# Performance work log

Measured on AMD Instinct MI355X. Metric: run time of the kernel, lower is better.

Reference implementation:

```python
import jax, jax.numpy as jnp
from jax import lax
import numpy as np

B, T, C_IN, H, W = 2, 4, 128, 64, 64
D_MODEL, N_Q, N_POINTS, PATCH, N_LAYERS = 256, 300, 8, 3, 6


def _sine_pos(Hh, Ww, d, temperature=10000.0):
    # mask is all-False, so cumsum of ones -> arange(1..H)/H * 2pi
    two_pi = 2.0 * np.pi
    yn = (jnp.arange(1, Hh + 1, dtype=jnp.float32) / (Hh + 1e-6)) * two_pi
    xn = (jnp.arange(1, Ww + 1, dtype=jnp.float32) / (Ww + 1e-6)) * two_pi
    q = d // 4
    i = jnp.arange(q, dtype=jnp.float32)
    dim_t = temperature ** (2.0 * jnp.floor(i / 2.0) / q)
    py = yn[:, None] / dim_t
    px = xn[:, None] / dim_t
    py = jnp.stack([jnp.sin(py), jnp.cos(py)], axis=-1).reshape(Hh, 2 * q)
    px = jnp.stack([jnp.sin(px), jnp.cos(px)], axis=-1).reshape(Ww, 2 * q)
    pos = jnp.concatenate([
        jnp.broadcast_to(py[:, None, :], (Hh, Ww, 2 * q)),
        jnp.broadcast_to(px[None, :, :], (Hh, Ww, 2 * q)),
    ], axis=-1)
    return jnp.transpose(pos, (2, 0, 1))  # [d,H,W]


def _sample_scale(fmap, ref, ps):
    # fmap [B,C,h,w]; ref [B,nQ,nP,2] in [0,1]. Bilinear grid_sample,
    # padding_mode='border', align_corners=True -> direct gather (no replication).
    Bc, C, h, w = fmap.shape
    half = (ps - 1) / 2.0
    off = jnp.linspace(-half, half, ps, dtype=jnp.float32)
    oy, ox = jnp.meshgrid(off, off, indexing='ij')  # [ps,ps]
    gx = ref[..., 0, None, None] * 2.0 - 1.0 + ox * (2.0 / w)  # [B,nQ,nP,ps,ps]
    gy = ref[..., 1, None, None] * 2.0 - 1.0 + oy * (2.0 / h)
    x = jnp.clip((gx + 1.0) * 0.5 * (w - 1), 0.0, w - 1.0)
    y = jnp.clip((gy + 1.0) * 0.5 * (h - 1), 0.0, h - 1.0)
    x0 = jnp.floor(x); y0 = jnp.floor(y)
    wx = x - x0; wy = y - y0
    x0i = x0.astype(jnp.int32); y0i = y0.astype(jnp.int32)
    x1i = jnp.minimum(x0i + 1, w - 1); y1i = jnp.minimum(y0i + 1, h - 1)

    def per_b(fb, y0b, x0b, y1b, x1b, wxb, wyb):
        v00 = fb[:, y0b, x0b]  # [C,nQ,nP,ps,ps]
        v01 = fb[:, y0b, x1b]
        v10 = fb[:, y1b, x0b]
        v11 = fb[:, y1b, x1b]
        return (v00 * (1 - wxb) * (1 - wyb) + v01 * wxb * (1 - wyb)
                + v10 * (1 - wxb) * wyb + v11 * wxb * wyb)

    out = jax.vmap(per_b)(fmap, y0i, x0i, y1i, x1i, wx, wy)  # [B,C,nQ,nP,ps,ps]
    return jnp.transpose(out, (0, 2, 3, 4, 5, 1))  # [B,nQ,nP,ps,ps,C]


def reference(feat, pred_boxes_init, w_tf, b_tf, w_in, b_in, w_lat, b_lat, w_sm, b_sm,
              q_embed, q_pos, Wq, bq, Wo, bo, Wp1, bp1, Wp2, bp2,
              w_r1, b_r1, w_r2, b_r2, w_b1, b_b1, w_b2, b_b2, w_cls, b_cls):
    Bb, Tt, Cin, Hh, Ww = feat.shape
    d = w_in.shape[0]
    nP = w_r2.shape[0] // 2
    ps = int(round((Wp1.shape[-1] // d) ** 0.5))
    # temporal fuse: Conv3d kernel (3,1,1), padding (1,0,0)
    x = lax.conv_general_dilated(jnp.transpose(feat, (0, 2, 1, 3, 4)), w_tf,
                                 (1, 1, 1), [(1, 1), (0, 0), (0, 0)],
                                 dimension_numbers=('NCDHW', 'OIDHW', 'NCDHW'))
    x = x + b_tf[None, :, None, None, None]
    x = x.mean(axis=2)  # [B,Cin,H,W]
    x = jnp.einsum('bchw,dc->bdhw', x, w_in) + b_in[None, :, None, None]
    x = x + _sine_pos(Hh, Ww, d)[None]
    # FPN over scales {1,2,4}: avg_pool -> 1x1 lateral -> 3x3 smooth
    feats = []
    for i, s in enumerate((1, 2, 4)):
        xi = x if s == 1 else x.reshape(Bb, d, Hh // s, s, Ww // s, s).mean(axis=(3, 5))
        xi = jnp.einsum('bchw,oc->bohw', xi, w_lat[i]) + b_lat[i][None, :, None, None]
        xi = lax.conv_general_dilated(xi, w_sm[i], (1, 1), [(1, 1), (1, 1)],
                                      dimension_numbers=('NCHW', 'OIHW', 'NCHW'))
        xi = xi + b_sm[i][None, :, None, None]
        feats.append(xi)
    nQ = q_embed.shape[0]
    queries = jnp.broadcast_to((q_embed + q_pos)[None], (Bb, nQ, d))
    boxes = pred_boxes_init
    inv_sqrt_d = 1.0 / float(np.sqrt(d))
    for l in range(Wq.shape[0]):
        h1 = jax.nn.relu(jnp.einsum('bqd,od->bqo', queries, w_r1) + b_r1)
        ro = jnp.tanh(jnp.einsum('bqd,od->bqo', h1, w_r2) + b_r2)
        ro = ro.reshape(Bb, nQ, nP, 2) * 0.5
        ref = jnp.clip(boxes[:, :, None, :2] + ro, 0.0, 1.0)
        sampled = jnp.concatenate([_sample_scale(f, ref, ps) for f in feats], axis=2)
        sampled = sampled[:, :, :nP]  # truncate multi-scale concat back to nP
        flat = sampled.reshape(Bb, nQ, nP, ps * ps * d)
        pv = jax.nn.relu(jnp.einsum('bqpi,oi->bqpo', flat, Wp1[l]) + bp1[l])
        pv = jnp.einsum('bqpd,od->bqpo', pv, Wp2[l]) + bp2[l]
        kv = pv.mean(axis=2)  # [B,nP_q,d] -> [B,nQ,d]
        q = jnp.einsum('bqd,od->bqo', queries, Wq[l]) + bq[l]
        attn = jax.nn.softmax(jnp.einsum('bqd,bkd->bqk', q, kv) * inv_sqrt_d, axis=-1)
        out = jnp.einsum('bqk,bkd->bqd', attn, kv)
        queries = queries + (jnp.einsum('bqd,od->bqo', out, Wo[l]) + bo[l])
        hb = jax.nn.relu(jnp.einsum('bqd,od->bqo', queries, w_b1) + b_b1)
        delta = jax.nn.sigmoid(jnp.einsum('bqd,od->bqo', hb, w_b2) + b_b2)
        boxes = jnp.clip(boxes + 0.1 * jnp.tanh(delta - 0.5), 0.0, 1.0)
    logits = (jnp.einsum('bqd,od->bqo', queries, w_cls) + b_cls)[..., 0]
    return logits, boxes


def setup_inputs() -> dict:
    key = jax.random.key(0)
    keys = iter(jax.random.split(key, 48))

    def nrm(shape, s=0.02):
        return jax.random.normal(next(keys), shape, dtype=jnp.float32) * s

    inp = {
        'feat': jax.random.normal(next(keys), (B, T, C_IN, H, W), dtype=jnp.float32),
        'pred_boxes_init': jax.random.uniform(next(keys), (B, N_Q, 4), dtype=jnp.float32),
        'w_tf': nrm((C_IN, C_IN, 3, 1, 1)), 'b_tf': jnp.zeros((C_IN,), jnp.float32),
        'w_in': nrm((D_MODEL, C_IN)), 'b_in': jnp.zeros((D_MODEL,), jnp.float32),
        'w_lat': nrm((3, D_MODEL, D_MODEL)), 'b_lat': jnp.zeros((3, D_MODEL), jnp.float32),
        'w_sm': nrm((3, D_MODEL, D_MODEL, 3, 3)), 'b_sm': jnp.zeros((3, D_MODEL), jnp.float32),
        'q_embed': nrm((N_Q, D_MODEL), 1.0), 'q_pos': nrm((N_Q, D_MODEL), 1.0),
        'Wq': nrm((N_LAYERS, D_MODEL, D_MODEL)), 'bq': jnp.zeros((N_LAYERS, D_MODEL), jnp.float32),
        'Wo': nrm((N_LAYERS, D_MODEL, D_MODEL)), 'bo': jnp.zeros((N_LAYERS, D_MODEL), jnp.float32),
        'Wp1': nrm((N_LAYERS, D_MODEL, PATCH * PATCH * D_MODEL)), 'bp1': jnp.zeros((N_LAYERS, D_MODEL), jnp.float32),
        'Wp2': nrm((N_LAYERS, D_MODEL, D_MODEL)), 'bp2': jnp.zeros((N_LAYERS, D_MODEL), jnp.float32),
        'w_r1': nrm((D_MODEL, D_MODEL)), 'b_r1': jnp.zeros((D_MODEL,), jnp.float32),
        'w_r2': nrm((2 * N_POINTS, D_MODEL)), 'b_r2': jnp.zeros((2 * N_POINTS,), jnp.float32),
        'w_b1': nrm((D_MODEL, D_MODEL)), 'b_b1': jnp.zeros((D_MODEL,), jnp.float32),
        'w_b2': nrm((4, D_MODEL)), 'b_b2': jnp.zeros((4,), jnp.float32),
        'w_cls': nrm((1, D_MODEL)), 'b_cls': jnp.zeros((1,), jnp.float32),
    }
    return inp
```

## Files before the change

kernel.cpp:

```cpp
#include <hip/hip_runtime.h>
#include <hip/hip_bf16.h>
#include <math.h>

#define BB 2
#define TT 4
#define CIN 128
#define DM 256
#define NQ 300
#define NP 8
#define PS 3
#define NL 6
#define HW 4096
#define KP 2304

typedef __attribute__((ext_vector_type(8))) short short8;
typedef __attribute__((ext_vector_type(4))) short short4_t;
typedef __attribute__((ext_vector_type(4))) float f32x4;
typedef unsigned short ushort_t;

static __device__ __forceinline__ ushort_t f2bf(float f) {
  __hip_bfloat16 h = __float2bfloat16(f);
  return *reinterpret_cast<ushort_t*>(&h);
}
static __device__ __forceinline__ float bf2f(ushort_t u) {
  return __uint_as_float(((unsigned)u) << 16);
}

__global__ void k_prep(const float* __restrict__ w_in, const float* __restrict__ w_lat,
                       const float* __restrict__ w_b1,
                       const float* __restrict__ w_r1, const float* __restrict__ Wp1,
                       ushort_t* __restrict__ win_bf, ushort_t* __restrict__ wlat_bf,
                       ushort_t* __restrict__ wb1_bf,
                       ushort_t* __restrict__ wr1_bf, ushort_t* __restrict__ wp1_bf,
                       const float* __restrict__ w_tf, ushort_t* __restrict__ tct,
                       const float* __restrict__ w_sm, ushort_t* __restrict__ wsm_bf,
                       const float* __restrict__ Wp2, const float* __restrict__ Wo,
                       const float* __restrict__ bq, const float* __restrict__ bp2,
                       const float* __restrict__ bo,
                       float* __restrict__ bqt, float* __restrict__ bfuse,
                       uint4* __restrict__ x2p_zero,
                       const float* __restrict__ b_tf, const float* __restrict__ b_in,
                       float* __restrict__ bias_comb,
                       const float* __restrict__ qe, const float* __restrict__ qp,
                       const float* __restrict__ pb, float* __restrict__ queries,
                       ushort_t* __restrict__ qbf, float* __restrict__ boxes,
                       const float* __restrict__ feat, ushort_t* __restrict__ featT) {
  __shared__ float ldsF[64][65];
  float* bt = &ldsF[0][0];
  int b = blockIdx.x, t = threadIdx.x;
  if (b < 3680) {
    int i = b * 256 + t;
    const float* s; ushort_t* d; int base;
    if (i < 8192)         { s = w_in;  d = win_bf;  base = 0; }
    else if (i < 24576)   { s = w_lat; d = wlat_bf; base = 8192; }
    else if (i < 40960)   { s = w_b1;  d = wb1_bf;  base = 24576; }
    else if (i < 57344)   { s = w_r1;  d = wr1_bf;  base = 40960; }
    else                  { s = Wp1;   d = wp1_bf;  base = 57344; }
    int j = i - base;
    float4 v = ((const float4*)s)[j];
    short4_t o;
    o[0] = (short)f2bf(v.x); o[1] = (short)f2bf(v.y);
    o[2] = (short)f2bf(v.z); o[3] = (short)f2bf(v.w);
    *(short4_t*)(d + j * 4) = o;
  } else if (b < 3936) {
    int i = (b - 3680) * 256 + t;
    int k = i >> 7, c = i & 127;
    int u = k >> 7, ci = k & 127;
    const float* wp = w_tf + ((size_t)(c * 128 + ci)) * 3;
    float w0 = wp[0], w1 = wp[1], w2 = wp[2];
    float coef = (u == 0) ? (w0 + w1) : (u == 3) ? (w1 + w2) : (w0 + w1 + w2);
    tct[(size_t)k * 128 + c] = f2bf(0.25f * coef);
  } else if (b < 4192) {
    int n = b - 3936;
    float* l2 = &ldsF[0][0];
    const float* src = w_sm + (size_t)n * KP;
    for (int idx = t; idx < 576; idx += 256) {
      float4 v = ((const float4*)src)[idx];
      l2[idx * 4 + 0] = v.x; l2[idx * 4 + 1] = v.y;
      l2[idx * 4 + 2] = v.z; l2[idx * 4 + 3] = v.w;
    }
    __syncthreads();
    ushort_t* dst = wsm_bf + (size_t)n * KP;
#pragma unroll
    for (int tp = 0; tp < 9; ++tp)
      dst[tp * 256 + t] = f2bf(l2[t * 9 + tp]);
  } else if (b < 4204) {
    int i = (b - 4192) * 256 + t;
    if (i < 1536) {
      int l = i >> 8, d = i & 255;
      float a = 0.f;
      for (int o = 0; o < 256; ++o)
        a += bq[l * 256 + o] * Wp2[((size_t)(l * 256 + o)) * 256 + d];
      bqt[i] = a;
    } else {
      int j = i - 1536;
      int l = j >> 8, o2 = j & 255;
      float a = bo[l * 256 + o2];
      for (int o = 0; o < 256; ++o)
        a += bp2[l * 256 + o] * Wo[((size_t)(l * 256 + o2)) * 256 + o];
      bfuse[j] = a;
    }
  } else if (b < 5293) {
    int j = (b - 4204) * 256 + t;
    if (j < 278784) x2p_zero[j] = make_uint4(0u, 0u, 0u, 0u);
  } else if (b < 5294) {
    int d = t;
    if (d < 128) bt[d] = b_tf[d];
    __syncthreads();
    float a = b_in[d];
    for (int c = 0; c < 128; ++c) a += w_in[d * 128 + c] * bt[c];
    bias_comb[d] = a;
  } else if (b < 5894) {
    int i = (b - 5294) * 256 + t;
    if (i < BB * NQ * DM) {
      int rd = i % (NQ * DM);
      float v = qe[rd] + qp[rd];
      queries[i] = v;
      qbf[i] = f2bf(v);
    }
    if (i < BB * NQ * 4) boxes[i] = pb[i];
  } else {
    int idx = b - 5894;
    int gs = idx & 127;
    int k0 = (idx >> 7) * 64;
    int bb = gs >> 6;
    int s0 = (gs & 63) * 64;
    int kk = t >> 2, sc0 = (t & 3) * 16;
    {
      int k = k0 + kk;
      int u = k >> 7, ci = k & 127;
      const float* src = feat + (((size_t)(bb * 4 + u) * 128 + ci) << 12) + s0 + sc0;
#pragma unroll
      for (int j = 0; j < 4; ++j) {
        float4 v = *(const float4*)(src + j * 4);
        ldsF[kk][sc0 + j * 4 + 0] = v.x;
        ldsF[kk][sc0 + j * 4 + 1] = v.y;
        ldsF[kk][sc0 + j * 4 + 2] = v.z;
        ldsF[kk][sc0 + j * 4 + 3] = v.w;
      }
    }
    __syncthreads();
#pragma unroll
    for (int p = 0; p < 2; ++p) {
      int idx2 = p * 256 + t;
      int s_l = idx2 >> 3, kc = (idx2 & 7) * 8;
      short8 v;
#pragma unroll
      for (int j = 0; j < 8; ++j) v[j] = (short)f2bf(ldsF[kc + j][s_l]);
      *(short8*)(featT + (size_t)(bb * 4096 + s0 + s_l) * 512 + k0 + kc) = v;
    }
  }
}

__global__ __launch_bounds__(256) void k_wcompose(const float* __restrict__ Wp2,
                                                  const float* __restrict__ Wq,
                                                  const float* __restrict__ Wo,
                                                  ushort_t* __restrict__ wqt,
                                                  ushort_t* __restrict__ wfuseT) {
  __shared__ ushort_t As[64 * 36];
  __shared__ ushort_t Bs[64 * 36];
  int z = blockIdx.z, l = z % 6;
  const float* Asrc = Wp2 + (size_t)l * 65536;
  const float* Bsrc = ((z < 6) ? Wq : Wo) + (size_t)l * 65536;
  ushort_t* C = ((z < 6) ? wqt : wfuseT) + (size_t)l * 65536;
  bool btr = (z < 6);
  int tid = threadIdx.x;
  int bm = blockIdx.x * 64, bn = blockIdx.y * 64;
  int w = tid >> 6, lane = tid & 63;
  int wm = (w & 1) * 32, wn = (w >> 1) * 32;
  int q = lane >> 4, ml = lane & 15;
  f32x4 acc[2][2] = {};
  int oo = tid >> 3, mg = (tid & 7) * 8;
  int nr = tid >> 2, kg = (tid & 3) * 8;
  for (int k0 = 0; k0 < 256; k0 += 32) {
    {
      const float* sp = Asrc + (size_t)(k0 + oo) * 256 + bm + mg;
      float4 f0 = *(const float4*)sp;
      float4 f1 = *(const float4*)(sp + 4);
      ushort_t* dst = As + oo;
      dst[(mg + 0) * 36] = f2bf(f0.x); dst[(mg + 1) * 36] = f2bf(f0.y);
      dst[(mg + 2) * 36] = f2bf(f0.z); dst[(mg + 3) * 36] = f2bf(f0.w);
      dst[(mg + 4) * 36] = f2bf(f1.x); dst[(mg + 5) * 36] = f2bf(f1.y);
      dst[(mg + 6) * 36] = f2bf(f1.z); dst[(mg + 7) * 36] = f2bf(f1.w);
    }
    if (btr) {
      const float* sp = Bsrc + (size_t)(k0 + oo) * 256 + bn + mg;
      float4 f0 = *(const float4*)sp;
      float4 f1 = *(const float4*)(sp + 4);
      ushort_t* dst = Bs + oo;
      dst[(mg + 0) * 36] = f2bf(f0.x); dst[(mg + 1) * 36] = f2bf(f0.y);
      dst[(mg + 2) * 36] = f2bf(f0.z); dst[(mg + 3) * 36] = f2bf(f0.w);
      dst[(mg + 4) * 36] = f2bf(f1.x); dst[(mg + 5) * 36] = f2bf(f1.y);
      dst[(mg + 6) * 36] = f2bf(f1.z); dst[(mg + 7) * 36] = f2bf(f1.w);
    } else {
      const float* sp = Bsrc + (size_t)(bn + nr) * 256 + k0 + kg;
      float4 f0 = *(const float4*)sp;
      float4 f1 = *(const float4*)(sp + 4);
      short8 v;
      v[0] = (short)f2bf(f0.x); v[1] = (short)f2bf(f0.y);
      v[2] = (short)f2bf(f0.z); v[3] = (short)f2bf(f0.w);
      v[4] = (short)f2bf(f1.x); v[5] = (short)f2bf(f1.y);
      v[6] = (short)f2bf(f1.z); v[7] = (short)f2bf(f1.w);
      *(short8*)(Bs + nr * 36 + kg) = v;
    }
    __syncthreads();
    short8 a0 = *(const short8*)(As + (wm + ml) * 36 + q * 8);
    short8 a1 = *(const short8*)(As + (wm + 16 + ml) * 36 + q * 8);
    short8 b0 = *(const short8*)(Bs + (wn + ml) * 36 + q * 8);
    short8 b1 = *(const short8*)(Bs + (wn + 16 + ml) * 36 + q * 8);
    acc[0][0] = __builtin_amdgcn_mfma_f32_16x16x32_bf16(a0, b0, acc[0][0], 0, 0, 0);
    acc[0][1] = __builtin_amdgcn_mfma_f32_16x16x32_bf16(a0, b1, acc[0][1], 0, 0, 0);
    acc[1][0] = __builtin_amdgcn_mfma_f32_16x16x32_bf16(a1, b0, acc[1][0], 0, 0, 0);
    acc[1][1] = __builtin_amdgcn_mfma_f32_16x16x32_bf16(a1, b1, acc[1][1], 0, 0, 0);
    __syncthreads();
  }
#pragma unroll
  for (int i = 0; i < 2; ++i)
#pragma unroll
    for (int j = 0; j < 2; ++j) {
      int cn = bn + wn + j * 16 + ml;
#pragma unroll
      for (int r = 0; r < 4; ++r) {
        int rm = bm + wm + i * 16 + q * 4 + r;
        C[(size_t)rm * 256 + cn] = f2bf(acc[i][j][r]);
      }
    }
}

__global__ __launch_bounds__(256) void k_feat2(const ushort_t* __restrict__ featT,
                                               const ushort_t* __restrict__ wcomb,
                                               const float* __restrict__ biasc,
                                               ushort_t* __restrict__ xcl) {
  __shared__ ushort_t As[32 * 72];
  __shared__ ushort_t Bs[64 * 72];
  __shared__ float dimt_s[256];
  int tid = threadIdx.x;
  {
    int dd = tid & 127;
    int ii = dd >> 1;
    dimt_s[tid] = powf(10000.0f, (2.0f * (float)(ii >> 1)) / 64.0f);
  }
  int bm = blockIdx.x * 32, bn = blockIdx.y * 64;
  int w = tid >> 6, lane = tid & 63;
  int wm = (w & 1) * 16, wn = (w >> 1) * 32;
  int q = lane >> 4, ml = lane & 15;
  int sra = tid >> 3, sca = (tid & 7) * 8;
  int srb = tid >> 2, scb = (tid & 3) * 16;
  const ushort_t* Ag = featT + (size_t)(bm + sra) * 512 + sca;
  const ushort_t* Wg = wcomb + (size_t)(bn + srb) * 512 + scb;
  f32x4 acc[2] = {};
  short8 av = *(const short8*)Ag;
  short8 wv0 = *(const short8*)Wg;
  short8 wv1 = *(const short8*)(Wg + 8);
  for (int k0 = 0; k0 < 512; k0 += 64) {
    *(short8*)(As + sra * 72 + sca) = av;
    *(short8*)(Bs + srb * 72 + scb) = wv0;
    *(short8*)(Bs + srb * 72 + scb + 8) = wv1;
    __syncthreads();
    if (k0 + 64 < 512) {
      av = *(const short8*)(Ag + k0 + 64);
      wv0 = *(const short8*)(Wg + k0 + 64);
      wv1 = *(const short8*)(Wg + k0 + 72);
    }
#pragma unroll
    for (int h = 0; h < 2; ++h) {
      int kc = h * 32 + q * 8;
      short8 a = *(const short8*)(As + (wm + ml) * 72 + kc);
      short8 b0 = *(const short8*)(Bs + (wn + ml) * 72 + kc);
      short8 b1 = *(const short8*)(Bs + (wn + 16 + ml) * 72 + kc);
      acc[0] = __builtin_amdgcn_mfma_f32_16x16x32_bf16(a, b0, acc[0], 0, 0, 0);
      acc[1] = __builtin_amdgcn_mfma_f32_16x16x32_bf16(a, b1, acc[1], 0, 0, 0);
    }
    __syncthreads();
  }
  const float FKT = 6.28318530717958647692f / 64.000001f;
#pragma unroll
  for (int j = 0; j < 2; ++j) {
    int cn = bn + wn + j * 16 + ml;
    float dimt = dimt_s[cn];
    float bC = biasc[cn];
    bool isx = cn >= 128;
    bool isc = cn & 1;
#pragma unroll
    for (int r = 0; r < 4; ++r) {
      int rm = bm + wm + q * 4 + r;
      int s = rm & 4095;
      int y = s >> 6, x = s & 63;
      float ang = (float)((isx ? x : y) + 1) * FKT / dimt;
      float pos = isc ? cosf(ang) : sinf(ang);
      xcl[(size_t)rm * 256 + cn] = f2bf(acc[j][r] + bC + pos);
    }
  }
}

template <int ACT, int OUTMODE, int MG>
__global__ __launch_bounds__(256) void k_gemm_bf16(const ushort_t* __restrict__ A,
                                                   const ushort_t* __restrict__ W,
                                                   const float* __restrict__ bias,
                                                   const float* __restrict__ res,
                                                   float* __restrict__ Cf,
                                                   ushort_t* __restrict__ Cb,
                                                   int M, int N, int K) {
  __shared__ ushort_t As[64 * 72];
  __shared__ ushort_t Bs[64 * 72];
  int tid = threadIdx.x;
  int bm = blockIdx.x * 64, bn = blockIdx.y * 64;
  int w = tid >> 6, lane = tid & 63;
  int wm = (w & 1) * 32, wn = (w >> 1) * 32;
  int q = lane >> 4, ml = lane & 15;
  f32x4 acc[2][2] = {};
  int srow = tid >> 2, scol = (tid & 3) * 16;
  int ga = bm + srow;
  if (MG) ga = min(ga, M - 1);
  const ushort_t* Ag = A + (size_t)ga * K + scol;
  const ushort_t* Wg = W + (size_t)(bn + srow) * K + scol;
  short8 av0 = *(const short8*)(Ag);
  short8 av1 = *(const short8*)(Ag + 8);
  short8 wv0 = *(const short8*)(Wg);
  short8 wv1 = *(const short8*)(Wg + 8);
  for (int k0 = 0; k0 < K; k0 += 64) {
    *(short8*)(As + srow * 72 + scol) = av0;
    *(short8*)(As + srow * 72 + scol + 8) = av1;
    *(short8*)(Bs + srow * 72 + scol) = wv0;
    *(short8*)(Bs + srow * 72 + scol + 8) = wv1;
    __syncthreads();
    if (k0 + 64 < K) {
      av0 = *(const short8*)(Ag + k0 + 64);
      av1 = *(const short8*)(Ag + k0 + 72);
      wv0 = *(const short8*)(Wg + k0 + 64);
      wv1 = *(const short8*)(Wg + k0 + 72);
    }
#pragma unroll
    for (int h = 0; h < 2; ++h) {
      int kc = h * 32 + q * 8;
      short8 a0 = *(const short8*)(As + (wm + ml) * 72 + kc);
      short8 a1 = *(const short8*)(As + (wm + 16 + ml) * 72 + kc);
      short8 b0 = *(const short8*)(Bs + (wn + ml) * 72 + kc);
      short8 b1 = *(const short8*)(Bs + (wn + 16 + ml) * 72 + kc);
      acc[0][0] = __builtin_amdgcn_mfma_f32_16x16x32_bf16(a0, b0, acc[0][0], 0, 0, 0);
      acc[0][1] = __builtin_amdgcn_mfma_f32_16x16x32_bf16(a0, b1, acc[0][1], 0, 0, 0);
      acc[1][0] = __builtin_amdgcn_mfma_f32_16x16x32_bf16(a1, b0, acc[1][0], 0, 0, 0);
      acc[1][1] = __builtin_amdgcn_mfma_f32_16x16x32_bf16(a1, b1, acc[1][1], 0, 0, 0);
    }
    __syncthreads();
  }
#pragma unroll
  for (int i = 0; i < 2; ++i) {
#pragma unroll
    for (int j = 0; j < 2; ++j) {
      int cn = bn + wn + j * 16 + ml;
      float bsv = bias ? bias[cn] : 0.f;
#pragma unroll
      for (int r = 0; r < 4; ++r) {
        int rm = bm + wm + i * 16 + q * 4 + r;
        if (MG && rm >= M) continue;
        float v = acc[i][j][r] + bsv;
        if (OUTMODE == 0) {
          if (ACT == 1) v = fmaxf(v, 0.f);
          Cf[(size_t)rm * N + cn] = v;
        } else if (OUTMODE == 1) {
          int b = rm >> 12, rem = rm & 4095;
          int y = rem >> 6, xx = rem & 63;
          Cb[(((size_t)(b * 66 + y + 1)) * 66 + xx + 1) * 256 + cn] = f2bf(v);
        } else if (OUTMODE == 6) {
          Cb[(size_t)rm * N + cn] = f2bf(v);
        }
      }
    }
  }
}

template <int OUTMODE>
__global__ __launch_bounds__(256) void k_gemm32(const ushort_t* __restrict__ A,
                                                const ushort_t* __restrict__ W,
                                                const float* __restrict__ bias,
                                                const float* __restrict__ res,
                                                float* __restrict__ Cf,
                                                ushort_t* __restrict__ Cb,
                                                int M, int K,
                                                const ushort_t* __restrict__ W2,
                                                const float* __restrict__ bias2,
                                                const ushort_t* __restrict__ W3,
                                                const float* __restrict__ bias3) {
  __shared__ ushort_t As[32 * 72];
  __shared__ ushort_t Bs[64 * 72];
  int tid = threadIdx.x;
  int bm = blockIdx.x * 32, bn = blockIdx.y * 64;
  int w = tid >> 6, lane = tid & 63;
  int wm = (w & 1) * 16, wn = (w >> 1) * 32;
  int q = lane >> 4, ml = lane & 15;
  int sra = tid >> 3, sca = (tid & 7) * 8;
  int srb = tid >> 2, scb = (tid & 3) * 16;
  int ga = min(bm + sra, M - 1);
  const ushort_t* Ag = A + (size_t)ga * K + sca;
  const ushort_t* Wg;
  if (OUTMODE == 7) {
    int seg = bn >> 8;
    const ushort_t* Wb = (seg == 0) ? W : ((seg == 1) ? W2 : W3);
    Wg = Wb + (size_t)((bn & 255) + srb) * K + scb;
  } else {
    const ushort_t* Wb = (bn < 256) ? W : W2;
    Wg = Wb + (size_t)((bn & 255) + srb) * K + scb;
  }
  f32x4 acc[2] = {};
  short8 av = *(const short8*)(Ag);
  short8 wv0 = *(const short8*)(Wg);
  short8 wv1 = *(const short8*)(Wg + 8);
  for (int k0 = 0; k0 < K; k0 += 64) {
    *(short8*)(As + sra * 72 + sca) = av;
    *(short8*)(Bs + srb * 72 + scb) = wv0;
    *(short8*)(Bs + srb * 72 + scb + 8) = wv1;
    __syncthreads();
    if (k0 + 64 < K) {
      av = *(const short8*)(Ag + k0 + 64);
      wv0 = *(const short8*)(Wg + k0 + 64);
      wv1 = *(const short8*)(Wg + k0 + 72);
    }
#pragma unroll
    for (int h = 0; h < 2; ++h) {
      int kc = h * 32 + q * 8;
      short8 a = *(const short8*)(As + (wm + ml) * 72 + kc);
      short8 b0 = *(const short8*)(Bs + (wn + ml) * 72 + kc);
      short8 b1 = *(const short8*)(Bs + (wn + 16 + ml) * 72 + kc);
      acc[0] = __builtin_amdgcn_mfma_f32_16x16x32_bf16(a, b0, acc[0], 0, 0, 0);
      acc[1] = __builtin_amdgcn_mfma_f32_16x16x32_bf16(a, b1, acc[1], 0, 0, 0);
    }
    __syncthreads();
  }
#pragma unroll
  for (int j = 0; j < 2; ++j) {
    int cn = bn + wn + j * 16 + ml;
    float bsv;
    if (OUTMODE == 7) {
      int seg = cn >> 8;
      bsv = ((seg == 0) ? bias : ((seg == 1) ? bias2 : bias3))[cn & 255];
    } else {
      bsv = ((cn < 256) ? bias : bias2)[cn & 255];
    }
#pragma unroll
    for (int r = 0; r < 4; ++r) {
      int rm = bm + wm + q * 4 + r;
      if (rm >= M) continue;
      float v = acc[j][r] + bsv;
      if (OUTMODE == 4) {
        if (cn < 256) Cf[(size_t)rm * 256 + cn] = fmaxf(v, 0.f);
        else Cb[(size_t)rm * 256 + (cn & 255)] = f2bf(v);
      } else {
        if (cn < 256) Cf[(size_t)rm * 256 + cn] = fmaxf(v, 0.f);
        else if (cn < 512) ((float*)Cb)[(size_t)rm * 256 + (cn & 255)] = fmaxf(v, 0.f);
        else ((ushort_t*)res)[(size_t)rm * 256 + (cn & 255)] = f2bf(v);
      }
    }
  }
}

__global__ __launch_bounds__(512) void k_wp1_split(const ushort_t* __restrict__ A,
                                                   const ushort_t* __restrict__ W,
                                                   ushort_t* __restrict__ part) {
  __shared__ ushort_t As[64 * 72];
  __shared__ ushort_t Bs[128 * 72];
  int tid = threadIdx.x;
  int bm = blockIdx.x * 64, bn = blockIdx.y * 128;
  int kz = blockIdx.z * 768;
  int w = tid >> 6, lane = tid & 63;
  int wm = (w & 1) * 32, wn = (w >> 1) * 32;
  int q = lane >> 4, ml = lane & 15;
  int srA = tid >> 3, scA = (tid & 7) * 8;
  int srB = tid >> 2, scB = (tid & 3) * 16;
  const ushort_t* Ag = A + (size_t)(bm + srA) * KP + kz + scA;
  const ushort_t* Wg = W + (size_t)(bn + srB) * KP + kz + scB;
  f32x4 acc[2][2] = {};
  short8 av = *(const short8*)(Ag);
  short8 wv0 = *(const short8*)(Wg);
  short8 wv1 = *(const short8*)(Wg + 8);
  for (int k0 = 0; k0 < 768; k0 += 64) {
    *(short8*)(As + srA * 72 + scA) = av;
    *(short8*)(Bs + srB * 72 + scB) = wv0;
    *(short8*)(Bs + srB * 72 + scB + 8) = wv1;
    __syncthreads();
    if (k0 + 64 < 768) {
      av = *(const short8*)(Ag + k0 + 64);
      wv0 = *(const short8*)(Wg + k0 + 64);
      wv1 = *(const short8*)(Wg + k0 + 72);
    }
#pragma unroll
    for (int h = 0; h < 2; ++h) {
      int kc = h * 32 + q * 8;
      short8 a0 = *(const short8*)(As + (wm + ml) * 72 + kc);
      short8 a1 = *(const short8*)(As + (wm + 16 + ml) * 72 + kc);
      short8 b0 = *(const short8*)(Bs + (wn + ml) * 72 + kc);
      short8 b1 = *(const short8*)(Bs + (wn + 16 + ml) * 72 + kc);
      acc[0][0] = __builtin_amdgcn_mfma_f32_16x16x32_bf16(a0, b0, acc[0][0], 0, 0, 0);
      acc[0][1] = __builtin_amdgcn_mfma_f32_16x16x32_bf16(a0, b1, acc[0][1], 0, 0, 0);
      acc[1][0] = __builtin_amdgcn_mfma_f32_16x16x32_bf16(a1, b0, acc[1][0], 0, 0, 0);
      acc[1][1] = __builtin_amdgcn_mfma_f32_16x16x32_bf16(a1, b1, acc[1][1], 0, 0, 0);
    }
    __syncthreads();
  }
  ushort_t* pz = part + (size_t)blockIdx.z * 4800 * 256;
#pragma unroll
  for (int i = 0; i < 2; ++i)
#pragma unroll
    for (int j = 0; j < 2; ++j) {
      int cn = bn + wn + j * 16 + ml;
#pragma unroll
      for (int r = 0; r < 4; ++r) {
        int rm = bm + wm + i * 16 + q * 4 + r;
        pz[(size_t)rm * 256 + cn] = f2bf(acc[i][j][r]);
      }
    }
}

__global__ __launch_bounds__(256) void k_wp1_reduce(const ushort_t* __restrict__ part,
                                                    const float* __restrict__ bias,
                                                    ushort_t* __restrict__ pvm) {
  int row = blockIdx.x;
  int d = threadIdx.x;
  float b = bias[d];
  float s = 0.f;
#pragma unroll
  for (int p = 0; p < 8; ++p) {
    size_t idx = (size_t)(row * 8 + p) * 256 + d;
    float v = bf2f(part[idx]) + bf2f(part[idx + (size_t)4800 * 256]) +
              bf2f(part[idx + (size_t)2 * 4800 * 256]) + b;
    s += fmaxf(v, 0.f);
  }
  pvm[(size_t)row * 256 + d] = f2bf(s * 0.125f);
}

__global__ __launch_bounds__(256) void k_conv3(const ushort_t* __restrict__ x2p,
                                               const ushort_t* __restrict__ wsm,
                                               const float* __restrict__ bsm,
                                               ushort_t* __restrict__ fcl) {
  __shared__ ushort_t As[32 * 72];
  __shared__ ushort_t Bs[64 * 72];
  int tid = threadIdx.x;
  int bm = blockIdx.x * 32, bn = blockIdx.y * 64;
  int w = tid >> 6, lane = tid & 63;
  int wm = (w & 1) * 16, wn = (w >> 1) * 32;
  int q = lane >> 4, ml = lane & 15;
  int sra = tid >> 3, sca = (tid & 7) * 8;
  int srb = tid >> 2, scb = (tid & 3) * 16;
  int sA = bm + sra;
  int b = sA >> 12, rem = sA & 4095;
  size_t pbase = ((size_t)(b * 66 + (rem >> 6)) * 66 + (rem & 63)) * 256;
  const ushort_t* Wg = wsm + (size_t)(bn + srb) * KP + scb;
  auto loadA = [&](int k0) {
    int ka = k0 + sca;
    int t9 = ka >> 8;
    int ky = t9 / 3, kx = t9 - ky * 3;
    return *(const short8*)(x2p + pbase + (size_t)(ky * 66 + kx) * 256 + (ka & 255));
  };
  f32x4 acc[2] = {};
  short8 av = loadA(0);
  short8 wv0 = *(const short8*)(Wg);
  short8 wv1 = *(const short8*)(Wg + 8);
  for (int k0 = 0; k0 < KP; k0 += 64) {
    *(short8*)(As + sra * 72 + sca) = av;
    *(short8*)(Bs + srb * 72 + scb) = wv0;
    *(short8*)(Bs + srb * 72 + scb + 8) = wv1;
    __syncthreads();
    if (k0 + 64 < KP) {
      av = loadA(k0 + 64);
      wv0 = *(const short8*)(Wg + k0 + 64);
      wv1 = *(const short8*)(Wg + k0 + 72);
    }
#pragma unroll
    for (int h = 0; h < 2; ++h) {
      int kc = h * 32 + q * 8;
      short8 a = *(const short8*)(As + (wm + ml) * 72 + kc);
      short8 b0 = *(const short8*)(Bs + (wn + ml) * 72 + kc);
      short8 b1 = *(const short8*)(Bs + (wn + 16 + ml) * 72 + kc);
      acc[0] = __builtin_amdgcn_mfma_f32_16x16x32_bf16(a, b0, acc[0], 0, 0, 0);
      acc[1] = __builtin_amdgcn_mfma_f32_16x16x32_bf16(a, b1, acc[1], 0, 0, 0);
    }
    __syncthreads();
  }
#pragma unroll
  for (int j = 0; j < 2; ++j) {
    int cn = bn + wn + j * 16 + ml;
    float bsv = bsm[cn];
#pragma unroll
    for (int r = 0; r < 4; ++r) {
      int rm = bm + wm + q * 4 + r;
      fcl[(size_t)rm * 256 + cn] = f2bf(acc[j][r] + bsv);
    }
  }
}

__global__ __launch_bounds__(256) void k_sample(const ushort_t* __restrict__ fcl,
                                                const float* __restrict__ h1,
                                                const float* __restrict__ w_r2,
                                                const float* __restrict__ b_r2,
                                                const float* __restrict__ boxesIn,
                                                float* __restrict__ boxesOut,
                                                const float* __restrict__ hb,
                                                const float* __restrict__ w_b2,
                                                const float* __restrict__ b_b2,
                                                ushort_t* __restrict__ flat) {
  __shared__ float pr[8];
  __shared__ float bc2[2];
  __shared__ float nb2[2];
  int blk = blockIdx.x;
  int row = blk >> 3, p = blk & 7;
  int b = row / NQ;
  int tid = threadIdx.x;
  int w = tid >> 6, lane = tid & 63;
  if (hb) {
    float4 hv = *(const float4*)(hb + (size_t)row * 256 + lane * 4);
    float4 wv = *(const float4*)(w_b2 + (size_t)w * 256 + lane * 4);
    float aa = hv.x * wv.x + hv.y * wv.y + hv.z * wv.z + hv.w * wv.w;
#pragma unroll
    for (int s = 32; s > 0; s >>= 1) aa += __shfl_down(aa, s, 64);
    if (lane == 0) {
      aa += b_b2[w];
      float delta = 1.0f / (1.0f + expf(-aa));
      float v = boxesIn[row * 4 + w] + 0.1f * tanhf(delta - 0.5f);
      v = fminf(fmaxf(v, 0.f), 1.f);
      if (w < 2) nb2[w] = v;
      if (p == 0) boxesOut[row * 4 + w] = v;
    }
  } else if (tid < 2) {
    nb2[tid] = boxesIn[row * 4 + tid];
  }
  float h = h1[(size_t)row * 256 + tid];
  float px = h * w_r2[(size_t)(2 * p) * 256 + tid];
  float py = h * w_r2[(size_t)(2 * p + 1) * 256 + tid];
#pragma unroll
  for (int s = 32; s > 0; s >>= 1) {
    px += __shfl_down(px, s, 64);
    py += __shfl_down(py, s, 64);
  }
  if (lane == 0) { pr[w * 2] = px; pr[w * 2 + 1] = py; }
  __syncthreads();
  if (tid == 0) {
    float sx = pr[0] + pr[2] + pr[4] + pr[6] + b_r2[2 * p];
    float sy = pr[1] + pr[3] + pr[5] + pr[7] + b_r2[2 * p + 1];
    float rx = nb2[0] + 0.5f * tanhf(sx);
    float ry = nb2[1] + 0.5f * tanhf(sy);
    bc2[0] = fminf(fmaxf(rx, 0.f), 1.f);
    bc2[1] = fminf(fmaxf(ry, 0.f), 1.f);
  }
  __syncthreads();
  float rx = bc2[0], ry = bc2[1];
  const ushort_t* fb = fcl + (size_t)b * HW * DM;
  ushort_t* op = flat + (size_t)blk * KP;
  int c4 = (tid & 63) * 4;
  int g = tid >> 6;
  int p0 = (g == 0) ? 0 : (1 + 2 * g);
  int p1 = (g == 0) ? 3 : (3 + 2 * g);
  for (int p9 = p0; p9 < p1; ++p9) {
    int jy = (p9 >= 6) ? 2 : ((p9 >= 3) ? 1 : 0);
    int jx = p9 - jy * 3;
    float yy = (ry + (float)(jy - 1) * (1.0f / 64.0f)) * 63.0f;
    yy = fminf(fmaxf(yy, 0.f), 63.0f);
    float y0f = floorf(yy);
    float wy = yy - y0f;
    int y0 = (int)y0f;
    int y1 = min(y0 + 1, 63);
    float xx = (rx + (float)(jx - 1) * (1.0f / 64.0f)) * 63.0f;
    xx = fminf(fmaxf(xx, 0.f), 63.0f);
    float x0f = floorf(xx);
    float wx = xx - x0f;
    int x0 = (int)x0f;
    int x1 = min(x0 + 1, 63);
    short4_t v00 = *(const short4_t*)(fb + (y0 * 64 + x0) * DM + c4);
    short4_t v01 = *(const short4_t*)(fb + (y0 * 64 + x1) * DM + c4);
    short4_t v10 = *(const short4_t*)(fb + (y1 * 64 + x0) * DM + c4);
    short4_t v11 = *(const short4_t*)(fb + (y1 * 64 + x1) * DM + c4);
    short4_t ov;
#pragma unroll
    for (int jj = 0; jj < 4; ++jj) {
      float v = bf2f((ushort_t)v00[jj]) * (1.f - wx) * (1.f - wy) +
                bf2f((ushort_t)v01[jj]) * wx * (1.f - wy) +
                bf2f((ushort_t)v10[jj]) * (1.f - wx) * wy +
                bf2f((ushort_t)v11[jj]) * wx * wy;
      ov[jj] = (short)f2bf(v);
    }
    *(short4_t*)(op + p9 * DM + c4) = ov;
  }
}

__global__ __launch_bounds__(256) void k_attn(const ushort_t* __restrict__ qt,
                                              const ushort_t* __restrict__ pvm,
                                              const ushort_t* __restrict__ wfT,
                                              const float* __restrict__ bfuse_l,
                                              float* __restrict__ queries,
                                              ushort_t* __restrict__ qbf) {
  __shared__ float qs[256];
  __shared__ float sc[512];
  __shared__ float red[256];
  __shared__ float pr4[1024];
  int row = blockIdx.x;
  int b = row / NQ;
  int tid = threadIdx.x;
  qs[tid] = bf2f(qt[(size_t)row * DM + tid]);
  __syncthreads();
  const ushort_t* kvB = pvm + (size_t)b * NQ * DM;
#pragma unroll
  for (int s2 = 0; s2 < 2; ++s2) {
    int k = tid + s2 * 256;
    float v = -1e30f;
    if (k < NQ) {
      const ushort_t* kp = kvB + (size_t)k * DM;
      float a = 0.f;
#pragma unroll
      for (int d = 0; d < 256; d += 8) {
        short8 k8 = *(const short8*)(kp + d);
        const float* qd = qs + d;
        a += bf2f((ushort_t)k8[0]) * qd[0];
        a += bf2f((ushort_t)k8[1]) * qd[1];
        a += bf2f((ushort_t)k8[2]) * qd[2];
        a += bf2f((ushort_t)k8[3]) * qd[3];
        a += bf2f((ushort_t)k8[4]) * qd[4];
        a += bf2f((ushort_t)k8[5]) * qd[5];
        a += bf2f((ushort_t)k8[6]) * qd[6];
        a += bf2f((ushort_t)k8[7]) * qd[7];
      }
      v = a * (1.0f / 16.0f);
    }
    sc[k] = v;
  }
  __syncthreads();
  red[tid] = fmaxf(sc[tid], sc[tid + 256]);
  __syncthreads();
  for (int st = 128; st > 0; st >>= 1) {
    if (tid < st) red[tid] = fmaxf(red[tid], red[tid + st]);
    __syncthreads();
  }
  float mx = red[0];
  __syncthreads();
  float e0 = (tid < NQ) ? expf(sc[tid] - mx) : 0.f;
  float e1 = (tid + 256 < NQ) ? expf(sc[tid + 256] - mx) : 0.f;
  sc[tid] = e0;
  sc[tid + 256] = e1;
  red[tid] = e0 + e1;
  __syncthreads();
  for (int st = 128; st > 0; st >>= 1) {
    if (tid < st) red[tid] += red[tid + st];
    __syncthreads();
  }
  float inv = 1.0f / red[0];
  __syncthreads();
  float acc = 0.f;
#pragma unroll 4
  for (int k = 0; k < NQ; ++k)
    acc += sc[k] * bf2f(kvB[(size_t)k * DM + tid]);
  qs[tid] = acc * inv;
  __syncthreads();
  int oq = (tid & 63) * 4, dq = (tid >> 6) * 64;
  float a0 = 0.f, a1 = 0.f, a2 = 0.f, a3 = 0.f;
  const ushort_t* wp = wfT + (size_t)dq * 256 + oq;
#pragma unroll 8
  for (int dd = 0; dd < 64; ++dd) {
    float cc = qs[dq + dd];
    short4_t wv = *(const short4_t*)(wp + (size_t)dd * 256);
    a0 += cc * bf2f((ushort_t)wv[0]);
    a1 += cc * bf2f((ushort_t)wv[1]);
    a2 += cc * bf2f((ushort_t)wv[2]);
    a3 += cc * bf2f((ushort_t)wv[3]);
  }
  float* pb4 = pr4 + (tid >> 6) * 256 + oq;
  pb4[0] = a0; pb4[1] = a1; pb4[2] = a2; pb4[3] = a3;
  __syncthreads();
  float v = pr4[tid] + pr4[256 + tid] + pr4[512 + tid] + pr4[768 + tid] +
            bfuse_l[tid] + queries[(size_t)row * DM + tid];
  queries[(size_t)row * DM + tid] = v;
  qbf[(size_t)row * DM + tid] = f2bf(v);
}

__global__ __launch_bounds__(256) void k_boxf(const float* __restrict__ hb,
                                              const float* __restrict__ w_b2,
                                              const float* __restrict__ b_b2,
                                              float* __restrict__ boxes,
                                              int last,
                                              const float* __restrict__ queries,
                                              const float* __restrict__ w_cls,
                                              const float* __restrict__ b_cls,
                                              float* __restrict__ out) {
  __shared__ float nb[4];
  int row = blockIdx.x;
  int tid = threadIdx.x;
  int j = tid >> 6, lane = tid & 63;
  float4 hv = *(const float4*)(hb + (size_t)row * 256 + lane * 4);
  float4 wv = *(const float4*)(w_b2 + (size_t)j * 256 + lane * 4);
  float aa = hv.x * wv.x + hv.y * wv.y + hv.z * wv.z + hv.w * wv.w;
#pragma unroll
  for (int s = 32; s > 0; s >>= 1) aa += __shfl_down(aa, s, 64);
  if (lane == 0) {
    aa += b_b2[j];
    float delta = 1.0f / (1.0f + expf(-aa));
    float v = boxes[row * 4 + j] + 0.1f * tanhf(delta - 0.5f);
    v = fminf(fmaxf(v, 0.f), 1.f);
    boxes[row * 4 + j] = v;
    nb[j] = v;
  }
  if (last) {
    __syncthreads();
    if (j == 0) {
      float4 qv = *(const float4*)(queries + (size_t)row * 256 + lane * 4);
      float4 cv = *(const float4*)(w_cls + lane * 4);
      float a2 = qv.x * cv.x + qv.y * cv.y + qv.z * cv.z + qv.w * cv.w;
#pragma unroll
      for (int s = 32; s > 0; s >>= 1) a2 += __shfl_down(a2, s, 64);
      if (lane == 0) out[row] = a2 + b_cls[0];
    } else if (j == 1 && lane < 4) {
      out[600 + row * 4 + lane] = nb[lane];
    }
  }
}

extern "C" void kernel_launch(void* const* d_in, const int* in_sizes, int n_in,
                              void* d_out, int out_size, void* d_ws, size_t ws_size,
                              hipStream_t stream) {
  const float* feat   = (const float*)d_in[0];
  const float* pb     = (const float*)d_in[1];
  const float* w_tf   = (const float*)d_in[2];
  const float* b_tf   = (const float*)d_in[3];
  const float* w_in   = (const float*)d_in[4];
  const float* b_in   = (const float*)d_in[5];
  const float* w_lat  = (const float*)d_in[6];
  const float* b_lat  = (const float*)d_in[7];
  const float* w_sm   = (const float*)d_in[8];
  const float* b_sm   = (const float*)d_in[9];
  const float* q_embed= (const float*)d_in[10];
  const float* q_pos  = (const float*)d_in[11];
  const float* Wq     = (const float*)d_in[12];
  const float* bq     = (const float*)d_in[13];
  const float* Wo     = (const float*)d_in[14];
  const float* bo     = (const float*)d_in[15];
  const float* Wp1    = (const float*)d_in[16];
  const float* bp1    = (const float*)d_in[17];
  const float* Wp2    = (const float*)d_in[18];
  const float* bp2    = (const float*)d_in[19];
  const float* w_r1   = (const float*)d_in[20];
  const float* b_r1   = (const float*)d_in[21];
  const float* w_r2   = (const float*)d_in[22];
  const float* b_r2   = (const float*)d_in[23];
  const float* w_b1   = (const float*)d_in[24];
  const float* b_b1   = (const float*)d_in[25];
  const float* w_b2   = (const float*)d_in[26];
  const float* b_b2   = (const float*)d_in[27];
  const float* w_cls  = (const float*)d_in[28];
  const float* b_cls  = (const float*)d_in[29];
  float* out = (float*)d_out;

  float* ws = (float*)d_ws;
  size_t off = 0;
  auto alloc = [&](size_t n) { float* p = ws + off; off += n; return p; };
  ushort_t* flat    = (ushort_t*)alloc(5529600);
  ushort_t* part    = (ushort_t*)alloc(1843200);
  ushort_t* featT   = (ushort_t*)alloc(2097152);
  ushort_t* xcl     = (ushort_t*)alloc(1048576);
  ushort_t* x2p     = (ushort_t*)alloc(1115136);
  ushort_t* fcl     = (ushort_t*)alloc(1048576);
  ushort_t* wcomb   = (ushort_t*)alloc(65536);
  ushort_t* tct     = (ushort_t*)alloc(32768);
  ushort_t* win_bf  = (ushort_t*)alloc(16384);
  float*    biasc   = alloc(256);
  ushort_t* wlat_bf = (ushort_t*)alloc(32768);
  ushort_t* wsm_bf  = (ushort_t*)alloc(294912);
  ushort_t* wp1_bf  = (ushort_t*)alloc(1769472);
  ushort_t* wb1_bf  = (ushort_t*)alloc(32768);
  ushort_t* wr1_bf  = (ushort_t*)alloc(32768);
  ushort_t* wqt_bf  = (ushort_t*)alloc(196608);
  ushort_t* wfuseT  = (ushort_t*)alloc(196608);
  float*    bqt     = alloc(1536);
  float*    bfuse   = alloc(1536);
  float* queries = alloc(153600);
  ushort_t* qbf  = (ushort_t*)alloc(76800);
  float* h1      = alloc(153600);
  ushort_t* qt   = (ushort_t*)alloc(76800);
  float* hb      = alloc(153600);
  ushort_t* pvm  = (ushort_t*)alloc(76800);
  float* boxesA  = alloc(2400);
  float* boxesB  = alloc(2400);
  (void)ws_size; (void)in_sizes; (void)n_in; (void)out_size;

  k_prep<<<6918, 256, 0, stream>>>(w_in, w_lat, w_b1, w_r1, Wp1,
                                   win_bf, wlat_bf, wb1_bf, wr1_bf, wp1_bf,
                                   w_tf, tct, w_sm, wsm_bf,
                                   Wp2, Wo, bq, bp2, bo, bqt, bfuse,
                                   (uint4*)x2p, b_tf, b_in, biasc,
                                   q_embed, q_pos, pb, queries, qbf, boxesA,
                                   feat, featT);
  k_gemm_bf16<0, 6, 0><<<dim3(4, 8), 256, 0, stream>>>(win_bf, tct, nullptr, nullptr,
                                                       nullptr, wcomb, 256, 512, 128);
  k_wcompose<<<dim3(4, 4, 12), 256, 0, stream>>>(Wp2, Wq, Wo, wqt_bf, wfuseT);

  k_feat2<<<dim3(256, 4), 256, 0, stream>>>(featT, wcomb, biasc, xcl);
  k_gemm_bf16<0, 1, 0><<<dim3(128, 4), 256, 0, stream>>>(xcl, wlat_bf, b_lat, nullptr,
                                                         nullptr, x2p, BB * HW, 256, 256);
  k_conv3<<<dim3(256, 4), 256, 0, stream>>>(x2p, wsm_bf, b_sm, fcl);

  const int M6 = BB * NQ;
  const int Mp = BB * NQ * NP;
  dim3 g600w((M6 + 31) / 32, 8);
  dim3 g600m((M6 + 31) / 32, 12);
  dim3 gsk(Mp / 64, 2, 3);

  k_gemm32<4><<<g600w, 256, 0, stream>>>(qbf, wr1_bf, b_r1, nullptr, h1,
                                         qt, M6, 256,
                                         wqt_bf, bqt, nullptr, nullptr);
  float* bcur = boxesA;
  float* bnext = boxesB;
  for (int l = 0; l < NL; ++l) {
    const float* hbp = (l == 0) ? nullptr : hb;
    k_sample<<<Mp, 256, 0, stream>>>(fcl, h1, w_r2, b_r2, bcur, bnext,
                                     hbp, w_b2, b_b2, flat);
    if (l > 0) { float* tmp = bcur; bcur = bnext; bnext = tmp; }
    k_wp1_split<<<gsk, 512, 0, stream>>>(flat, wp1_bf + (size_t)l * 256 * KP, part);
    k_wp1_reduce<<<600, 256, 0, stream>>>(part, bp1 + (size_t)l * DM, pvm);
    k_attn<<<M6, 256, 0, stream>>>(qt, pvm, wfuseT + (size_t)l * 65536,
                                   bfuse + l * 256, queries, qbf);
    int ln = (l + 1) % NL;
    k_gemm32<7><<<g600m, 256, 0, stream>>>(qbf, wb1_bf, b_b1, (const float*)qt,
                                           hb, (ushort_t*)h1, M6, 256,
                                           wr1_bf, b_r1,
                                           wqt_bf + (size_t)ln * 65536,
                                           bqt + ln * 256);
  }
  k_boxf<<<M6, 256, 0, stream>>>(hb, w_b2, b_b2, bcur, 1,
                                 queries, w_cls, b_cls, out);
}
```

Before: 647.0 us.

## Widen conv3 N tile to 128 and use wave-shuffle softmax reductions in attention

k_conv3 now runs 512 threads per block over a 128-wide output-channel tile, so each A tile is loaded once and reused across twice as many columns, halving the grid's y dimension. The A load is split into 4-element pieces across more threads. In k_attn, the shared-memory tree reductions for softmax max and sum are replaced by wave-level shuffle reductions plus a tiny cross-wave step, which removes many __syncthreads. Score values stay in registers instead of round-tripping through shared memory. The larger conv3 block raises LDS and register demand per block and may lower occupancy.

```diff
diff --git a/kernel.cpp b/kernel.cpp
--- a/kernel.cpp
+++ b/kernel.cpp
@@ -528,18 +528,18 @@
   pvm[(size_t)row * 256 + d] = f2bf(s * 0.125f);
 }
 
-__global__ __launch_bounds__(256) void k_conv3(const ushort_t* __restrict__ x2p,
+__global__ __launch_bounds__(512) void k_conv3(const ushort_t* __restrict__ x2p,
                                                const ushort_t* __restrict__ wsm,
                                                const float* __restrict__ bsm,
                                                ushort_t* __restrict__ fcl) {
   __shared__ ushort_t As[32 * 72];
-  __shared__ ushort_t Bs[64 * 72];
+  __shared__ ushort_t Bs[128 * 72];
   int tid = threadIdx.x;
-  int bm = blockIdx.x * 32, bn = blockIdx.y * 64;
+  int bm = blockIdx.x * 32, bn = blockIdx.y * 128;
   int w = tid >> 6, lane = tid & 63;
   int wm = (w & 1) * 16, wn = (w >> 1) * 32;
   int q = lane >> 4, ml = lane & 15;
-  int sra = tid >> 3, sca = (tid & 7) * 8;
+  int sra = tid >> 4, sca = (tid & 15) * 4;
   int srb = tid >> 2, scb = (tid & 3) * 16;
   int sA = bm + sra;
   int b = sA >> 12, rem = sA & 4095;
@@ -549,14 +549,14 @@
     int ka = k0 + sca;
     int t9 = ka >> 8;
     int ky = t9 / 3, kx = t9 - ky * 3;
-    return *(const short8*)(x2p + pbase + (size_t)(ky * 66 + kx) * 256 + (ka & 255));
+    return *(const short4_t*)(x2p + pbase + (size_t)(ky * 66 + kx) * 256 + (ka & 255));
   };
   f32x4 acc[2] = {};
-  short8 av = loadA(0);
+  short4_t av = loadA(0);
   short8 wv0 = *(const short8*)(Wg);
   short8 wv1 = *(const short8*)(Wg + 8);
   for (int k0 = 0; k0 < KP; k0 += 64) {
-    *(short8*)(As + sra * 72 + sca) = av;
+    *(short4_t*)(As + sra * 72 + sca) = av;
     *(short8*)(Bs + srb * 72 + scb) = wv0;
     *(short8*)(Bs + srb * 72 + scb + 8) = wv1;
     __syncthreads();
@@ -689,59 +689,68 @@
                                               ushort_t* __restrict__ qbf) {
   __shared__ float qs[256];
   __shared__ float sc[512];
-  __shared__ float red[256];
+  __shared__ float red[8];
   __shared__ float pr4[1024];
   int row = blockIdx.x;
   int b = row / NQ;
   int tid = threadIdx.x;
+  int w = tid >> 6, lane = tid & 63;
   qs[tid] = bf2f(qt[(size_t)row * DM + tid]);
   __syncthreads();
   const ushort_t* kvB = pvm + (size_t)b * NQ * DM;
-#pragma unroll
-  for (int s2 = 0; s2 < 2; ++s2) {
-    int k = tid + s2 * 256;
-    float v = -1e30f;
-    if (k < NQ) {
-      const ushort_t* kp = kvB + (size_t)k * DM;
-      float a = 0.f;
-#pragma unroll
-      for (int d = 0; d < 256; d += 8) {
-        short8 k8 = *(const short8*)(kp + d);
-        const float* qd = qs + d;
-        a += bf2f((ushort_t)k8[0]) * qd[0];
-        a += bf2f((ushort_t)k8[1]) * qd[1];
-        a += bf2f((ushort_t)k8[2]) * qd[2];
-        a += bf2f((ushort_t)k8[3]) * qd[3];
-        a += bf2f((ushort_t)k8[4]) * qd[4];
-        a += bf2f((ushort_t)k8[5]) * qd[5];
-        a += bf2f((ushort_t)k8[6]) * qd[6];
-        a += bf2f((ushort_t)k8[7]) * qd[7];
-      }
-      v = a * (1.0f / 16.0f);
-    }
-    sc[k] = v;
-  }
+  float v0, v1 = -1e30f;
+  {
+    const ushort_t* kp = kvB + (size_t)tid * DM;
+    float a = 0.f;
+#pragma unroll
+    for (int d = 0; d < 256; d += 8) {
+      short8 k8 = *(const short8*)(kp + d);
+      const float* qd = qs + d;
+      a += bf2f((ushort_t)k8[0]) * qd[0];
+      a += bf2f((ushort_t)k8[1]) * qd[1];
+      a += bf2f((ushort_t)k8[2]) * qd[2];
+      a += bf2f((ushort_t)k8[3]) * qd[3];
+      a += bf2f((ushort_t)k8[4]) * qd[4];
+      a += bf2f((ushort_t)k8[5]) * qd[5];
+      a += bf2f((ushort_t)k8[6]) * qd[6];
+      a += bf2f((ushort_t)k8[7]) * qd[7];
+    }
+    v0 = a * (1.0f / 16.0f);
+  }
+  if (tid + 256 < NQ) {
+    const ushort_t* kp = kvB + (size_t)(tid + 256) * DM;
+    float a = 0.f;
+#pragma unroll
+    for (int d = 0; d < 256; d += 8) {
+      short8 k8 = *(const short8*)(kp + d);
+      const float* qd = qs + d;
+      a += bf2f((ushort_t)k8[0]) * qd[0];
+      a += bf2f((ushort_t)k8[1]) * qd[1];
+      a += bf2f((ushort_t)k8[2]) * qd[2];
+      a += bf2f((ushort_t)k8[3]) * qd[3];
+      a += bf2f((ushort_t)k8[4]) * qd[4];
+      a += bf2f((ushort_t)k8[5]) * qd[5];
+      a += bf2f((ushort_t)k8[6]) * qd[6];
+      a += bf2f((ushort_t)k8[7]) * qd[7];
+    }
+    v1 = a * (1.0f / 16.0f);
+  }
+  float m = fmaxf(v0, v1);
+#pragma unroll
+  for (int s = 32; s > 0; s >>= 1) m = fmaxf(m, __shfl_xor(m, s, 64));
+  if (lane == 0) red[w] = m;
   __syncthreads();
-  red[tid] = fmaxf(sc[tid], sc[tid + 256]);
-  __syncthreads();
-  for (int st = 128; st > 0; st >>= 1) {
-    if (tid < st) red[tid] = fmaxf(red[tid], red[tid + st]);
-    __syncthreads();
-  }
-  float mx = red[0];
-  __syncthreads();
-  float e0 = (tid < NQ) ? expf(sc[tid] - mx) : 0.f;
-  float e1 = (tid + 256 < NQ) ? expf(sc[tid + 256] - mx) : 0.f;
+  float mx = fmaxf(fmaxf(red[0], red[1]), fmaxf(red[2], red[3]));
+  float e0 = expf(v0 - mx);
+  float e1 = (tid + 256 < NQ) ? expf(v1 - mx) : 0.f;
   sc[tid] = e0;
   sc[tid + 256] = e1;
-  red[tid] = e0 + e1;
+  float s = e0 + e1;
+#pragma unroll
+  for (int st = 32; st > 0; st >>= 1) s += __shfl_xor(s, st, 64);
+  if (lane == 0) red[4 + w] = s;
   __syncthreads();
-  for (int st = 128; st > 0; st >>= 1) {
-    if (tid < st) red[tid] += red[tid + st];
-    __syncthreads();
-  }
-  float inv = 1.0f / red[0];
-  __syncthreads();
+  float inv = 1.0f / (red[4] + red[5] + red[6] + red[7]);
   float acc = 0.f;
 #pragma unroll 4
   for (int k = 0; k < NQ; ++k)
@@ -891,7 +900,7 @@
   k_feat2<<<dim3(256, 4), 256, 0, stream>>>(featT, wcomb, biasc, xcl);
   k_gemm_bf16<0, 1, 0><<<dim3(128, 4), 256, 0, stream>>>(xcl, wlat_bf, b_lat, nullptr,
                                                          nullptr, x2p, BB * HW, 256, 256);
-  k_conv3<<<dim3(256, 4), 256, 0, stream>>>(x2p, wsm_bf, b_sm, fcl);
+  k_conv3<<<dim3(256, 2), 512, 0, stream>>>(x2p, wsm_bf, b_sm, fcl);
 
   const int M6 = BB * NQ;
   const int Mp = BB * NQ * NP;
```

After: 839.2 us. +29.7%, slower.
